# Kernel tuning notes

Hardware: AMD Instinct MI355X
Metric: run time of the kernel (lower is better)

The kernel has to match this reference:

```python
import jax, jax.numpy as jnp
import numpy as np


def setup_inputs() -> dict:
    key = jax.random.key(0)
    inputs = jax.random.normal(key, (64, 4096, 256), dtype=jnp.float32)
    return {"inputs": inputs}


def reference(inputs) -> jnp.ndarray:
    # inputs: [B, N, D]; tfp.stats.covariance(sample_axis=1) -> population cov [B, D, D]
    B, N, D = inputs.shape
    mean = jnp.mean(inputs, axis=1, keepdims=True)            # [B, 1, D]
    xc = inputs - mean                                        # centered samples
    cov = jnp.einsum('bnd,bne->bde', xc, xc) / N              # [B, D, D]
    # band_part(ones, 0, -1) keeps the UPPER triangle (incl. diagonal);
    # boolean_mask flattens row-major -> triu entries in row-major order.
    iu, ju = jnp.triu_indices(D)
    return cov[:, iu, ju]                                     # [B, D*(D+1)//2]
```

## Files before the change

kernel.cpp:

```cpp
#include <hip/hip_runtime.h>
#include <hip/hip_bf16.h>
#include <stdint.h>

typedef unsigned short u16;
typedef unsigned int   u32;

#define NB   64
#define NN   4096
#define ND   256
#define NTRI 32896
#define NSPLIT 4
#define KROWS  1024
#define NCHUNK 16

__device__ __forceinline__ u32 cvtpk(float lo, float hi) {
  u32 r;
  asm("v_cvt_pk_bf16_f32 %0, %1, %2" : "=v"(r) : "v"(lo), "v"(hi));
  return r;
}

typedef __attribute__((ext_vector_type(8))) __bf16 bf16x8;
typedef __attribute__((ext_vector_type(4))) float  f32x4;

__global__ __launch_bounds__(768) void k_cov(const float* __restrict__ in,
                                             float* __restrict__ covp,
                                             float* __restrict__ part) {
  __shared__ alignas(16) u16 Lt[2][2][256][32];
  __shared__ float msum[8][256];

  int blk = blockIdx.x;
  int b = blk >> 2, s = blk & 3;
  int t = threadIdx.x;
  int w = t >> 6, lane = t & 63;

  int tsel = w >> 2;
  int quad = w & 3;
  int wr = quad >> 1, wc = quad & 1;
  int ti = (tsel == 2) ? 1 : 0;
  int tj = (tsel == 0) ? 0 : 1;
  bool diag = (ti == tj);
  bool alive = !(diag && quad == 2);
  int fr = lane & 15, fg = lane >> 4;
  int dpA = ti * 128 + wr * 64;
  int dpB = tj * 128 + wc * 64;

  int aoffB[4], boffB[4];
  int jj = (fg ^ (fr >> 2)) << 4;
#pragma unroll
  for (int m = 0; m < 4; ++m) aoffB[m] = (dpA + m * 16 + fr) * 64 + jj;
#pragma unroll
  for (int n = 0; n < 4; ++n) boffB[n] = (dpB + n * 16 + fr) * 64 + jj;

  bool stager = (w < 8);
  int c4 = lane;
  int ksw = w >> 2;
  int xw = w & 3;
  int swz = ((xw ^ (c4 & 3)) << 4);

  f32x4 acc[4][4];
  f32x4 zero = {0.f, 0.f, 0.f, 0.f};
#pragma unroll
  for (int m = 0; m < 4; ++m)
#pragma unroll
    for (int n = 0; n < 4; ++n) acc[m][n] = zero;

  const float4* in4 = (const float4*)(in + (size_t)b * NN * ND);
  int rbase0 = (s * KROWS + w * 8) * 64 + c4;

  float4 ms = make_float4(0.f, 0.f, 0.f, 0.f);
  float4 s0, s1, s2, s3, s4, s5, s6, s7;
  uint4 q0, q1, q2, q3;

#define ISSUE(C)                                                \
  if (stager && (C) < NCHUNK) {                                 \
    int rb = rbase0 + (C) * 4096;                               \
    s0 = in4[rb + 0 * 64]; s1 = in4[rb + 1 * 64];               \
    s2 = in4[rb + 2 * 64]; s3 = in4[rb + 3 * 64];               \
    s4 = in4[rb + 4 * 64]; s5 = in4[rb + 5 * 64];               \
    s6 = in4[rb + 6 * 64]; s7 = in4[rb + 7 * 64];               \
  }

#define CVT()                                                                 \
  if (stager) {                                                               \
    ms.x += s0.x + s1.x + s2.x + s3.x + s4.x + s5.x + s6.x + s7.x;            \
    ms.y += s0.y + s1.y + s2.y + s3.y + s4.y + s5.y + s6.y + s7.y;            \
    ms.z += s0.z + s1.z + s2.z + s3.z + s4.z + s5.z + s6.z + s7.z;            \
    ms.w += s0.w + s1.w + s2.w + s3.w + s4.w + s5.w + s6.w + s7.w;            \
    q0 = make_uint4(cvtpk(s0.x, s1.x), cvtpk(s2.x, s3.x),                     \
                    cvtpk(s4.x, s5.x), cvtpk(s6.x, s7.x));                    \
    q1 = make_uint4(cvtpk(s0.y, s1.y), cvtpk(s2.y, s3.y),                     \
                    cvtpk(s4.y, s5.y), cvtpk(s6.y, s7.y));                    \
    q2 = make_uint4(cvtpk(s0.z, s1.z), cvtpk(s2.z, s3.z),                     \
                    cvtpk(s4.z, s5.z), cvtpk(s6.z, s7.z));                    \
    q3 = make_uint4(cvtpk(s0.w, s1.w), cvtpk(s2.w, s3.w),                     \
                    cvtpk(s4.w, s5.w), cvtpk(s6.w, s7.w));                    \
  }

#define WRITE(BUF)                                                            \
  if (stager) {                                                               \
    char* pl = (char*)&Lt[BUF][ksw][0][0] + swz;                              \
    *(uint4*)(pl + (c4 * 4 + 0) * 64) = q0;                                   \
    *(uint4*)(pl + (c4 * 4 + 1) * 64) = q1;                                   \
    *(uint4*)(pl + (c4 * 4 + 2) * 64) = q2;                                   \
    *(uint4*)(pl + (c4 * 4 + 3) * 64) = q3;                                   \
  }

#define COMPUTE(BUF)                                                          \
  if (alive) {                                                                \
    _Pragma("unroll")                                                         \
    for (int ks = 0; ks < 2; ++ks) {                                          \
      const char* pl = (const char*)&Lt[BUF][ks][0][0];                       \
      bf16x8 af[4], bfv[4];                                                   \
      _Pragma("unroll")                                                       \
      for (int m = 0; m < 4; ++m) af[m] = *(const bf16x8*)(pl + aoffB[m]);    \
      _Pragma("unroll")                                                       \
      for (int n = 0; n < 4; ++n) bfv[n] = *(const bf16x8*)(pl + boffB[n]);   \
      _Pragma("unroll")                                                       \
      for (int m = 0; m < 4; ++m)                                             \
        _Pragma("unroll")                                                     \
        for (int n = 0; n < 4; ++n)                                           \
          acc[m][n] = __builtin_amdgcn_mfma_f32_16x16x32_bf16(                \
              af[m], bfv[n], acc[m][n], 0, 0, 0);                             \
    }                                                                         \
  }

  ISSUE(0);
  CVT();
  ISSUE(1);
  WRITE(0);
  __syncthreads();
  for (int c = 0; c < NCHUNK - 1; ++c) {
    CVT();
    ISSUE(c + 2);
    WRITE((c + 1) & 1);
    COMPUTE(c & 1);
    __syncthreads();
  }
  COMPUTE((NCHUNK - 1) & 1);

  if (stager) *(float4*)&msum[w][c4 * 4] = ms;
  __syncthreads();
  if (t < 256) {
    float m = 0.f;
#pragma unroll
    for (int q = 0; q < 8; ++q) m += msum[q][t];
    part[(size_t)(b * 4 + s) * 256 + t] = m;
  }

  if (alive) {
    float* cp = covp + ((size_t)(s * 192 + b * 3 + tsel) << 14);
#pragma unroll
    for (int m = 0; m < 4; ++m)
#pragma unroll
      for (int q = 0; q < 4; ++q) {
        int li = wr * 64 + m * 16 + fg * 4 + q;
#pragma unroll
        for (int n = 0; n < 4; ++n) {
          int lj = wc * 64 + n * 16 + fr;
          cp[li * 128 + lj] = acc[m][n][q];
        }
      }
  }
#undef ISSUE
#undef CVT
#undef WRITE
#undef COMPUTE
}

__global__ __launch_bounds__(256) void k_fin(const float* __restrict__ covp,
                                             const float* __restrict__ part,
                                             float* __restrict__ out) {
  __shared__ float mean_s[256];
  int blk = blockIdx.x;
  int tile = blk >> 1, half = blk & 1;
  int b = tile / 3, tsel = tile % 3;
  int ti = (tsel == 2) ? 1 : 0;
  int tj = (tsel == 0) ? 0 : 1;
  int t = threadIdx.x;

  float m = 0.f;
#pragma unroll
  for (int q = 0; q < NSPLIT; ++q) m += part[(size_t)(b * 4 + q) * 256 + t];
  mean_s[t] = m * (1.f / 4096.f);
  __syncthreads();

  const float4* cp0 = (const float4*)(covp + ((size_t)(0 * 192 + tile) << 14));
  const float4* cp1 = (const float4*)(covp + ((size_t)(1 * 192 + tile) << 14));
  const float4* cp2 = (const float4*)(covp + ((size_t)(2 * 192 + tile) << 14));
  const float4* cp3 = (const float4*)(covp + ((size_t)(3 * 192 + tile) << 14));

  float* ob = out + (size_t)b * NTRI;
  for (int e4 = t; e4 < 2048; e4 += 256) {
    int e = half * 8192 + (e4 << 2);
    int li = e >> 7, lj0 = e & 127;
    int i = ti * 128 + li;
    if (tj * 128 + lj0 + 3 < i) continue;
    int q = e >> 2;
    float4 v0 = cp0[q], v1 = cp1[q], v2 = cp2[q], v3 = cp3[q];
    float sum[4] = {v0.x + v1.x + v2.x + v3.x, v0.y + v1.y + v2.y + v3.y,
                    v0.z + v1.z + v2.z + v3.z, v0.w + v1.w + v2.w + v3.w};
    float mi = mean_s[i];
    int ro = i * 256 - ((i * (i - 1)) >> 1) - i;
#pragma unroll
    for (int k = 0; k < 4; ++k) {
      int j = tj * 128 + lj0 + k;
      if (j >= i)
        ob[ro + j] = sum[k] * (1.f / 4096.f) - mi * mean_s[j];
    }
  }
}

__global__ __launch_bounds__(256) void k_cov_f32(const float* __restrict__ in,
                                                 float* __restrict__ out) {
  int blk = blockIdx.x;
  int b = blk / 10, ts = blk % 10;
  int ti, tj;
  if (ts < 4)      { ti = 0; tj = ts; }
  else if (ts < 7) { ti = 1; tj = ts - 3; }
  else if (ts < 9) { ti = 2; tj = ts - 5; }
  else             { ti = 3; tj = 3; }
  bool diag = (ti == tj);

  __shared__ float Pa[32][68];
  __shared__ float Pb[32][68];
  __shared__ float smA[64], smB[64];
  int t = threadIdx.x;
  if (t < 64) { smA[t] = 0.f; smB[t] = 0.f; }
  float acc[4][4] = {};
  int ri = t >> 4, rj = t & 15;
  const float* base = in + (size_t)b * NN * ND;

  for (int ks = 0; ks < 128; ++ks) {
    int nk = ks * 32;
    __syncthreads();
    for (int cc = t; cc < 512; cc += 256) {
      int r = cc >> 4, c4 = (cc & 15) << 2;
      *(float4*)&Pa[r][c4] = *(const float4*)(base + (size_t)(nk + r) * ND + ti * 64 + c4);
      if (!diag)
        *(float4*)&Pb[r][c4] = *(const float4*)(base + (size_t)(nk + r) * ND + tj * 64 + c4);
    }
    __syncthreads();
    if (t < 64) {
      float s = 0.f;
      for (int r = 0; r < 32; ++r) s += Pa[r][t];
      smA[t] += s;
    } else if (!diag && t < 128) {
      float s = 0.f;
      for (int r = 0; r < 32; ++r) s += Pb[r][t - 64];
      smB[t - 64] += s;
    }
    float(*Pbb)[68] = diag ? Pa : Pb;
    for (int k = 0; k < 32; ++k) {
      float4 a = *(const float4*)&Pa[k][ri << 2];
      float4 v = *(const float4*)&Pbb[k][rj << 2];
      float av[4] = {a.x, a.y, a.z, a.w};
      float bv[4] = {v.x, v.y, v.z, v.w};
#pragma unroll
      for (int e = 0; e < 4; ++e)
#pragma unroll
        for (int f = 0; f < 4; ++f) acc[e][f] += av[e] * bv[f];
    }
  }
  __syncthreads();
  const float inv = 1.f / 4096.f;
  const float* mB = diag ? smA : smB;
#pragma unroll
  for (int e = 0; e < 4; ++e) {
    int i = ti * 64 + (ri << 2) + e;
    float mi = smA[(ri << 2) + e] * inv;
    int ro = i * 256 - ((i * (i - 1)) >> 1) - i;
#pragma unroll
    for (int f = 0; f < 4; ++f) {
      int j = tj * 64 + (rj << 2) + f;
      if (j >= i)
        out[(size_t)b * NTRI + ro + j] = acc[e][f] * inv - mi * mB[(rj << 2) + f] * inv;
    }
  }
}

extern "C" void kernel_launch(void* const* d_in, const int* in_sizes, int n_in,
                              void* d_out, int out_size, void* d_ws, size_t ws_size,
                              hipStream_t stream) {
  const float* in = (const float*)d_in[0];
  float* out = (float*)d_out;

  const size_t COVP_B = (size_t)NSPLIT * 192 * 16384 * 4;
  const size_t PART_B = (size_t)NB * NSPLIT * 256 * 4;
  const size_t need = COVP_B + PART_B;

  if (ws_size >= need) {
    float* covp = (float*)d_ws;
    float* part = (float*)((char*)d_ws + COVP_B);
    k_cov<<<NB * NSPLIT, 768, 0, stream>>>(in, covp, part);
    k_fin<<<NB * 3 * 2, 256, 0, stream>>>(covp, part, out);
  } else {
    k_cov_f32<<<NB * 10, 256, 0, stream>>>(in, out);
  }
}
```

Measured before the change: 70.30 us.

## Prefetch two input chunks ahead using alternating A/B register sets

The staging loop is restructured so two sets of register buffers (A for even chunks, B for odd) keep two global-load chunks in flight instead of one. The loop is unrolled by two, with conversion and LDS writes fused into one step, and scheduling barriers keep each next load from being moved above the MFMA compute. This is meant to hide more global-memory latency behind the matrix work. In exchange it doubles the staging register footprint on the stager waves at 768 threads per block, which may raise register pressure or cause spills.

```diff
diff --git a/kernel.cpp b/kernel.cpp
--- a/kernel.cpp
+++ b/kernel.cpp
@@ -68,42 +68,50 @@
   int rbase0 = (s * KROWS + w * 8) * 64 + c4;
 
   float4 ms = make_float4(0.f, 0.f, 0.f, 0.f);
-  float4 s0, s1, s2, s3, s4, s5, s6, s7;
-  uint4 q0, q1, q2, q3;
-
-#define ISSUE(C)                                                \
-  if (stager && (C) < NCHUNK) {                                 \
+  float4 a0, a1, a2, a3, a4, a5, a6, a7;
+  float4 b0, b1, b2, b3, b4, b5, b6, b7;
+
+#define ISSUE_A(C)                                              \
+  if (stager) {                                                 \
     int rb = rbase0 + (C) * 4096;                               \
-    s0 = in4[rb + 0 * 64]; s1 = in4[rb + 1 * 64];               \
-    s2 = in4[rb + 2 * 64]; s3 = in4[rb + 3 * 64];               \
-    s4 = in4[rb + 4 * 64]; s5 = in4[rb + 5 * 64];               \
-    s6 = in4[rb + 6 * 64]; s7 = in4[rb + 7 * 64];               \
-  }
-
-#define CVT()                                                                 \
+    a0 = in4[rb + 0 * 64]; a1 = in4[rb + 1 * 64];               \
+    a2 = in4[rb + 2 * 64]; a3 = in4[rb + 3 * 64];               \
+    a4 = in4[rb + 4 * 64]; a5 = in4[rb + 5 * 64];               \
+    a6 = in4[rb + 6 * 64]; a7 = in4[rb + 7 * 64];               \
+  }
+
+#define ISSUE_B(C)                                              \
+  if (stager) {                                                 \
+    int rb = rbase0 + (C) * 4096;                               \
+    b0 = in4[rb + 0 * 64]; b1 = in4[rb + 1 * 64];               \
+    b2 = in4[rb + 2 * 64]; b3 = in4[rb + 3 * 64];               \
+    b4 = in4[rb + 4 * 64]; b5 = in4[rb + 5 * 64];               \
+    b6 = in4[rb + 6 * 64]; b7 = in4[rb + 7 * 64];               \
+  }
+
+#define CVT_WRITE(BUF, r0, r1, r2, r3, r4, r5, r6, r7)                        \
   if (stager) {                                                               \
-    ms.x += s0.x + s1.x + s2.x + s3.x + s4.x + s5.x + s6.x + s7.x;            \
-    ms.y += s0.y + s1.y + s2.y + s3.y + s4.y + s5.y + s6.y + s7.y;            \
-    ms.z += s0.z + s1.z + s2.z + s3.z + s4.z + s5.z + s6.z + s7.z;            \
-    ms.w += s0.w + s1.w + s2.w + s3.w + s4.w + s5.w + s6.w + s7.w;            \
-    q0 = make_uint4(cvtpk(s0.x, s1.x), cvtpk(s2.x, s3.x),                     \
-                    cvtpk(s4.x, s5.x), cvtpk(s6.x, s7.x));                    \
-    q1 = make_uint4(cvtpk(s0.y, s1.y), cvtpk(s2.y, s3.y),                     \
-                    cvtpk(s4.y, s5.y), cvtpk(s6.y, s7.y));                    \
-    q2 = make_uint4(cvtpk(s0.z, s1.z), cvtpk(s2.z, s3.z),                     \
-                    cvtpk(s4.z, s5.z), cvtpk(s6.z, s7.z));                    \
-    q3 = make_uint4(cvtpk(s0.w, s1.w), cvtpk(s2.w, s3.w),                     \
-                    cvtpk(s4.w, s5.w), cvtpk(s6.w, s7.w));                    \
-  }
-
-#define WRITE(BUF)                                                            \
-  if (stager) {                                                               \
+    ms.x += r0.x + r1.x + r2.x + r3.x + r4.x + r5.x + r6.x + r7.x;            \
+    ms.y += r0.y + r1.y + r2.y + r3.y + r4.y + r5.y + r6.y + r7.y;            \
+    ms.z += r0.z + r1.z + r2.z + r3.z + r4.z + r5.z + r6.z + r7.z;            \
+    ms.w += r0.w + r1.w + r2.w + r3.w + r4.w + r5.w + r6.w + r7.w;            \
     char* pl = (char*)&Lt[BUF][ksw][0][0] + swz;                              \
-    *(uint4*)(pl + (c4 * 4 + 0) * 64) = q0;                                   \
-    *(uint4*)(pl + (c4 * 4 + 1) * 64) = q1;                                   \
-    *(uint4*)(pl + (c4 * 4 + 2) * 64) = q2;                                   \
-    *(uint4*)(pl + (c4 * 4 + 3) * 64) = q3;                                   \
-  }
+    *(uint4*)(pl + (c4 * 4 + 0) * 64) =                                       \
+      make_uint4(cvtpk(r0.x, r1.x), cvtpk(r2.x, r3.x),                        \
+                 cvtpk(r4.x, r5.x), cvtpk(r6.x, r7.x));                       \
+    *(uint4*)(pl + (c4 * 4 + 1) * 64) =                                       \
+      make_uint4(cvtpk(r0.y, r1.y), cvtpk(r2.y, r3.y),                        \
+                 cvtpk(r4.y, r5.y), cvtpk(r6.y, r7.y));                       \
+    *(uint4*)(pl + (c4 * 4 + 2) * 64) =                                       \
+      make_uint4(cvtpk(r0.z, r1.z), cvtpk(r2.z, r3.z),                        \
+                 cvtpk(r4.z, r5.z), cvtpk(r6.z, r7.z));                       \
+    *(uint4*)(pl + (c4 * 4 + 3) * 64) =                                       \
+      make_uint4(cvtpk(r0.w, r1.w), cvtpk(r2.w, r3.w),                        \
+                 cvtpk(r4.w, r5.w), cvtpk(r6.w, r7.w));                       \
+  }
+
+#define CVT_WRITE_A() CVT_WRITE(0, a0, a1, a2, a3, a4, a5, a6, a7)
+#define CVT_WRITE_B() CVT_WRITE(1, b0, b1, b2, b3, b4, b5, b6, b7)
 
 #define COMPUTE(BUF)                                                          \
   if (alive) {                                                                \
@@ -124,19 +132,24 @@
     }                                                                         \
   }
 
-  ISSUE(0);
-  CVT();
-  ISSUE(1);
-  WRITE(0);
+  ISSUE_A(0);
+  ISSUE_B(1);
+  CVT_WRITE_A();
+  ISSUE_A(2);
   __syncthreads();
-  for (int c = 0; c < NCHUNK - 1; ++c) {
-    CVT();
-    ISSUE(c + 2);
-    WRITE((c + 1) & 1);
-    COMPUTE(c & 1);
+
+  for (int c = 0; c < NCHUNK; c += 2) {
+    CVT_WRITE_B();
+    COMPUTE(0);
+    __builtin_amdgcn_sched_barrier(0);
+    if (c + 3 < NCHUNK) ISSUE_B(c + 3);
     __syncthreads();
-  }
-  COMPUTE((NCHUNK - 1) & 1);
+    if (c + 2 < NCHUNK) CVT_WRITE_A();
+    COMPUTE(1);
+    __builtin_amdgcn_sched_barrier(0);
+    if (c + 4 < NCHUNK) ISSUE_A(c + 4);
+    __syncthreads();
+  }
 
   if (stager) *(float4*)&msum[w][c4 * 4] = ms;
   __syncthreads();
@@ -161,9 +174,11 @@
         }
       }
   }
-#undef ISSUE
-#undef CVT
-#undef WRITE
+#undef ISSUE_A
+#undef ISSUE_B
+#undef CVT_WRITE
+#undef CVT_WRITE_A
+#undef CVT_WRITE_B
 #undef COMPUTE
 }
 
```

After: 71.06 us. Within noise of the previous version (+1.1%).
